# Kernel optimization log

Measured on AMD Instinct MI355X. Metric: run time of the kernel, lower is better.

Reference implementation:

```python
import jax, jax.numpy as jnp
import numpy as np

EPS_NORM = 1e-12
EPS_COS = 1e-8

def _l2norm(x, axis):
    n = jnp.linalg.norm(x, axis=axis, keepdims=True)
    return x / jnp.maximum(n, EPS_NORM)

def setup_inputs() -> dict:
    key = jax.random.key(0)
    k1, k2, k3 = jax.random.split(key, 3)
    B, C, H, W, M = 16, 512, 32, 32, 1024
    query = jax.random.normal(k1, (B, C, H, W), dtype=jnp.float32)
    keys = jax.random.normal(k2, (M, C), dtype=jnp.float32)
    entropy = jax.random.uniform(k3, (B * H * W, 1), dtype=jnp.float32) + 1e-3
    return {"query": query, "keys": keys, "entropy": entropy}

def reference(query, keys, entropy):
    B, C, H, W = query.shape
    M = keys.shape[0]
    N = B * H * W
    # F.normalize over channel dim, then BCHW -> BHWC -> [N, C]
    q = _l2norm(query, axis=1)
    q = jnp.transpose(q, (0, 2, 3, 1))
    qr = q.reshape(N, C)

    # get_score: softmax over queries (axis 0) and over memory (axis 1)
    score = jnp.einsum('nd,md->nm', qr, keys)  # [N, M]
    sq = jax.nn.softmax(score, axis=0)
    sm = jax.nn.softmax(score, axis=1)

    # ---- memory_loss ----
    argm = jnp.argmax(sm, axis=1)               # topk(k=1) over memory
    closest = keys[argm]                         # [N, C]
    eye = jnp.eye(M, dtype=keys.dtype)
    gram = keys @ keys.T
    diversity_loss = jnp.sum((gram * (1.0 - eye)) ** 2) / (M * M - M)
    cos = jnp.sum(qr * closest, axis=1) / jnp.maximum(
        jnp.linalg.norm(qr, axis=1) * jnp.linalg.norm(closest, axis=1), EPS_COS)
    similarity_loss = jnp.dot(1.0 - cos, entropy[:, 0])  # CosineEmbeddingLoss(target=1) . entropy

    # ---- read ----
    concat_memory = jax.lax.stop_gradient(sm) @ keys    # [N, C]
    updated_query = jnp.concatenate([qr, concat_memory], axis=1)  # [N, 2C]
    updated_query = updated_query.reshape(B, H, W, 2 * C)
    updated_query = jnp.transpose(updated_query, (0, 3, 1, 2))    # [B, 2C, H, W]

    # ---- update (train=True) ----
    g = argm                                     # gathering indices (argmax == topk1)
    sq_d = jax.lax.stop_gradient(sq)
    ent_d = jax.lax.stop_gradient(entropy[:, 0])
    colmax = jnp.max(sq_d, axis=0)               # max score per memory slot [M]
    w = (sq_d[jnp.arange(N), g] / colmax[g]) * (ent_d / jnp.max(ent_d))  # [N]
    query_update = jax.ops.segment_sum(w[:, None] * qr, g, num_segments=M)  # [M, C]
    updated_memory = _l2norm(query_update + jax.lax.stop_gradient(keys), axis=1)
    gram2 = updated_memory @ updated_memory.T
    diversity_loss_updated = jnp.sum((gram2 * (1.0 - eye)) ** 2) / (M * M - M)
    updated_memory = jax.lax.stop_gradient(updated_memory)

    return (updated_query, updated_memory, sq, sm, diversity_loss_updated, similarity_loss)
```

## Files before the change

kernel.cpp:

```cpp
#include <hip/hip_runtime.h>

typedef unsigned int  u32;
typedef unsigned short u16;
typedef __bf16 bf16x8 __attribute__((ext_vector_type(8)));
typedef float  f32x4  __attribute__((ext_vector_type(4)));

#define O1 16777216
#define O2 17301504
#define O3 34078720
#define O4 50855936
#define O5 50855937

#define WS_QHI   0u
#define WS_QLO   16777216u
#define WS_KHI   33554432u
#define WS_KLO   34603008u
#define WS_KT    35651584u
#define WS_KNORM 36700160u
#define WS_CNT   36704256u
#define WS_OFFS  36708352u
#define WS_CUR   36712704u
#define WS_RN    36769792u
#define WS_PMAX  36835328u
#define WS_CMAX  36966400u
#define WS_CSUM  36970496u
#define WS_ARGM  36974592u
#define WS_WGT   37040128u
#define WS_SCAL  39202816u
#define WS_PM2   39203840u
#define WS_PS2   39728128u
#define WS_SM16  40252416u

__device__ __forceinline__ u16 bf_rne(float f){
  u32 u = __float_as_uint(f);
  u32 r = u + 0x7fffu + ((u >> 16) & 1u);
  return (u16)(r >> 16);
}
__device__ __forceinline__ float bf_f(u16 h){ return __uint_as_float(((u32)h) << 16); }

__device__ __forceinline__ void glds16(const void* g, void* l){
  __builtin_amdgcn_global_load_lds((const __attribute__((address_space(1))) u32*)g,
                                   (__attribute__((address_space(3))) u32*)l, 16, 0, 0);
}

__global__ void k_init(u32* count, float* scal){
  int i = blockIdx.x*256 + threadIdx.x;
  if (i < 1024) count[i] = 0u;
  if (i < 16) scal[i] = 0.f;
}

__global__ __launch_bounds__(64) void k_keys(const float* __restrict__ keys,
    u16* __restrict__ khi, u16* __restrict__ klo, float* __restrict__ knorm){
  int m = blockIdx.x, l = threadIdx.x;
  const float* kr = keys + (size_t)m*512 + l*8;
  float f[8];
  #pragma unroll
  for (int i=0;i<8;i++) f[i] = kr[i];
  float ss = 0.f;
  #pragma unroll
  for (int i=0;i<8;i++) ss += f[i]*f[i];
  for (int o=32;o>0;o>>=1) ss += __shfl_xor(ss,o);
  if (l == 0) knorm[m] = sqrtf(ss);
  u32 hh[4], ll[4];
  #pragma unroll
  for (int i=0;i<4;i++){
    u16 h0 = bf_rne(f[2*i]);   u16 l0 = bf_rne(f[2*i]   - bf_f(h0));
    u16 h1 = bf_rne(f[2*i+1]); u16 l1 = bf_rne(f[2*i+1] - bf_f(h1));
    hh[i] = (u32)h0 | ((u32)h1<<16);
    ll[i] = (u32)l0 | ((u32)l1<<16);
  }
  *(uint4*)&khi[(size_t)m*512 + l*8] = make_uint4(hh[0],hh[1],hh[2],hh[3]);
  *(uint4*)&klo[(size_t)m*512 + l*8] = make_uint4(ll[0],ll[1],ll[2],ll[3]);
}

__global__ __launch_bounds__(256) void k_keysT(const float* __restrict__ keys, u16* __restrict__ kT){
  __shared__ float t2[64*65];
  int m0 = blockIdx.x*64, c0 = blockIdx.y*64;
  int t = threadIdx.x; int j = t & 63; int ig = t >> 6;
  #pragma unroll 4
  for (int ii=0; ii<16; ++ii){
    int i = ig*16 + ii;
    t2[i*65 + j] = keys[(size_t)(m0+i)*512 + c0 + j];
  }
  __syncthreads();
  #pragma unroll 4
  for (int ii=0; ii<16; ++ii){
    int i = ig*16 + ii;
    kT[(size_t)(c0+i)*1024 + m0 + j] = bf_rne(t2[j*65 + i]);
  }
}

__global__ __launch_bounds__(256) void k_maxent(const float* __restrict__ ent, float* scal){
  int i = blockIdx.x*512 + threadIdx.x;
  float v = fmaxf(ent[i], ent[i + 256]);
  for (int o=32;o>0;o>>=1) v = fmaxf(v, __shfl_xor(v,o));
  __shared__ float r4[4];
  if ((threadIdx.x & 63) == 0) r4[threadIdx.x>>6] = v;
  __syncthreads();
  if (threadIdx.x == 0){
    float mx = fmaxf(fmaxf(r4[0],r4[1]), fmaxf(r4[2],r4[3]));
    atomicMax((u32*)(scal + 1), __float_as_uint(mx));
  }
}

__global__ __launch_bounds__(256) void k_phaseA(const float* __restrict__ query, float* __restrict__ out0,
    u16* __restrict__ qhi, u16* __restrict__ qlo, float* __restrict__ rn_g){
  __shared__ float tile[64*65];
  __shared__ float red[256];
  __shared__ float sinv[64];
  int bx = blockIdx.x; int b = bx >> 4; int hw0 = (bx & 15)*64;
  int t = threadIdx.x; int hw = t & 63; int cg = t >> 6;
  const float* qb = query + (size_t)b*524288 + hw0 + hw;
  float p = 0.f;
  for (int c = cg; c < 512; c += 4){ float v = qb[(size_t)c*1024]; p += v*v; }
  red[cg*64 + hw] = p;
  __syncthreads();
  if (t < 64){
    float ss = red[t] + red[64+t] + red[128+t] + red[192+t];
    float nrm = sqrtf(ss);
    float inv = 1.0f / fmaxf(nrm, 1e-12f);
    sinv[t] = inv;
    rn_g[b*1024 + hw0 + t] = nrm * inv;
  }
  __syncthreads();
  int nl = t >> 2, cq = t & 3;
  int n = b*1024 + hw0 + nl;
  float invv = sinv[hw];
  for (int cb = 0; cb < 8; ++cb){
    int cbase = cb*64;
    #pragma unroll 4
    for (int i = 0; i < 16; ++i){
      int cl = cg*16 + i;
      int c = cbase + cl;
      float v = query[(size_t)b*524288 + (size_t)c*1024 + hw0 + hw] * invv;
      tile[cl*65 + hw] = v;
      out0[(size_t)b*1048576 + (size_t)c*1024 + hw0 + hw] = v;
    }
    __syncthreads();
    u32 hh[8], ll[8];
    #pragma unroll
    for (int p2 = 0; p2 < 8; ++p2){
      float f0 = tile[(cq*16 + p2*2)*65 + nl];
      float f1 = tile[(cq*16 + p2*2 + 1)*65 + nl];
      u16 h0 = bf_rne(f0); u16 lo0 = bf_rne(f0 - bf_f(h0));
      u16 h1 = bf_rne(f1); u16 lo1 = bf_rne(f1 - bf_f(h1));
      hh[p2] = (u32)h0 | ((u32)h1 << 16);
      ll[p2] = (u32)lo0 | ((u32)lo1 << 16);
    }
    size_t base = (size_t)n*512 + cbase + cq*16;
    *(uint4*)&qhi[base]     = make_uint4(hh[0],hh[1],hh[2],hh[3]);
    *(uint4*)&qhi[base + 8] = make_uint4(hh[4],hh[5],hh[6],hh[7]);
    *(uint4*)&qlo[base]     = make_uint4(ll[0],ll[1],ll[2],ll[3]);
    *(uint4*)&qlo[base + 8] = make_uint4(ll[4],ll[5],ll[6],ll[7]);
    __syncthreads();
  }
}

__global__ __launch_bounds__(256) void k_score(const u16* __restrict__ qhi, const u16* __restrict__ qlo,
    const u16* __restrict__ khi, const u16* __restrict__ klo, float* __restrict__ S,
    float* __restrict__ pm2, float* __restrict__ ps2){
  __shared__ u16 sAh[8192], sAl[8192], sBh[8192], sBl[8192];
  int tid = threadIdx.x;
  int nt = blockIdx.x >> 3, mt = blockIdx.x & 7;
  int nBase = nt*128, mBase = mt*128;
  int wave = tid >> 6, lane = tid & 63;
  int rw = (wave>>1)*64, cw = (wave&1)*64;
  int m16 = lane & 15, q4 = lane >> 4;
  f32x4 acc[4][4] = {};
  int srow = tid >> 3, sg = tid & 7;
  for (int kit = 0; kit < 8; ++kit){
    int k0 = kit*64;
    #pragma unroll
    for (int it = 0; it < 4; ++it){
      int row = it*32 + srow;
      int gsw = (sg ^ (row & 7)) * 8;
      int lo = it*2048 + tid*8;
      glds16(qhi + (size_t)(nBase + row)*512 + k0 + gsw, &sAh[lo]);
      glds16(qlo + (size_t)(nBase + row)*512 + k0 + gsw, &sAl[lo]);
      glds16(khi + (size_t)(mBase + row)*512 + k0 + gsw, &sBh[lo]);
      glds16(klo + (size_t)(mBase + row)*512 + k0 + gsw, &sBl[lo]);
    }
    __syncthreads();
    #pragma unroll
    for (int ks = 0; ks < 2; ++ks){
      bf16x8 a0[4], a1[4], b0[4], b1[4];
      int g = ks*4 + q4;
      #pragma unroll
      for (int i=0;i<4;i++){
        int r = rw + i*16 + m16;
        int off = r*64 + (g ^ (r&7))*8;
        a0[i] = *(const bf16x8*)&sAh[off];
        a1[i] = *(const bf16x8*)&sAl[off];
      }
      #pragma unroll
      for (int j=0;j<4;j++){
        int r = cw + j*16 + m16;
        int off = r*64 + (g ^ (r&7))*8;
        b0[j] = *(const bf16x8*)&sBh[off];
        b1[j] = *(const bf16x8*)&sBl[off];
      }
      #pragma unroll
      for (int i=0;i<4;i++)
        #pragma unroll
        for (int j=0;j<4;j++){
          acc[i][j] = __builtin_amdgcn_mfma_f32_16x16x32_bf16(a0[i], b0[j], acc[i][j], 0,0,0);
          acc[i][j] = __builtin_amdgcn_mfma_f32_16x16x32_bf16(a0[i], b1[j], acc[i][j], 0,0,0);
          acc[i][j] = __builtin_amdgcn_mfma_f32_16x16x32_bf16(a1[i], b0[j], acc[i][j], 0,0,0);
        }
    }
    __syncthreads();
  }
  #pragma unroll
  for (int i=0;i<4;i++){
    int rbase = nBase + rw + i*16 + q4*4;
    #pragma unroll
    for (int j=0;j<4;j++){
      int col = mBase + cw + j*16 + m16;
      #pragma unroll
      for (int r=0;r<4;r++)
        S[(size_t)(rbase + r)*1024 + col] = acc[i][j][r];
    }
  }
  float* lm = (float*)sAh;
  float* ls = lm + 256;
  #pragma unroll
  for (int j=0;j<4;j++){
    float cm = -3.4e38f;
    #pragma unroll
    for (int i=0;i<4;i++)
      #pragma unroll
      for (int r=0;r<4;r++) cm = fmaxf(cm, acc[i][j][r]);
    cm = fmaxf(cm, __shfl_xor(cm, 16));
    cm = fmaxf(cm, __shfl_xor(cm, 32));
    float cs = 0.f;
    #pragma unroll
    for (int i=0;i<4;i++)
      #pragma unroll
      for (int r=0;r<4;r++) cs += __expf(acc[i][j][r] - cm);
    cs += __shfl_xor(cs, 16);
    cs += __shfl_xor(cs, 32);
    if (lane < 16){
      lm[(wave*4 + j)*16 + m16] = cm;
      ls[(wave*4 + j)*16 + m16] = cs;
    }
  }
  __syncthreads();
  if (tid < 128){
    int w = tid >> 6;
    int x = tid & 63;
    int j = x >> 4, c16 = x & 15;
    float m0 = lm[(w*4 + j)*16 + c16],     s0 = ls[(w*4 + j)*16 + c16];
    float m1 = lm[((w+2)*4 + j)*16 + c16], s1 = ls[((w+2)*4 + j)*16 + c16];
    float M  = fmaxf(m0, m1);
    float Sv = s0*__expf(m0 - M) + s1*__expf(m1 - M);
    int col = mBase + w*64 + j*16 + c16;
    pm2[nt*1024 + col] = M;
    ps2[nt*1024 + col] = Sv;
  }
}

__global__ void k_colfin(const float* __restrict__ pm2, const float* __restrict__ ps2,
    float* __restrict__ cmax, float* __restrict__ csum){
  int col = blockIdx.x*256 + threadIdx.x;
  float M = -3.4e38f, s = 0.f;
  for (int ch=0; ch<128; ++ch){
    float mi = pm2[ch*1024 + col], si = ps2[ch*1024 + col];
    float nm = fmaxf(M, mi);
    s = s*__expf(M - nm) + si*__expf(mi - nm);
    M = nm;
  }
  cmax[col] = M; csum[col] = s;
}

__global__ __launch_bounds__(256) void k_row(float* __restrict__ S, float* __restrict__ sm,
    u16* __restrict__ sm16,
    const float* __restrict__ cmax, const float* __restrict__ csum,
    const float* __restrict__ rn, const float* __restrict__ knorm,
    const float* __restrict__ ent, const float* __restrict__ scal,
    int* __restrict__ argm, float* __restrict__ wgt, u32* __restrict__ count,
    float* __restrict__ sim_acc){
  int wave = threadIdx.x >> 6, lane = threadIdx.x & 63;
  int n = blockIdx.x*4 + wave;
  float4 v[4];
  const float4* Sr = (const float4*)(S + (size_t)n*1024);
  #pragma unroll
  for (int j=0;j<4;j++) v[j] = Sr[j*64 + lane];
  float m = -3.4e38f; int gi = 0;
  #pragma unroll
  for (int j=0;j<4;j++){
    int c0 = j*256 + lane*4;
    if (v[j].x > m){ m=v[j].x; gi=c0; }
    if (v[j].y > m){ m=v[j].y; gi=c0+1; }
    if (v[j].z > m){ m=v[j].z; gi=c0+2; }
    if (v[j].w > m){ m=v[j].w; gi=c0+3; }
  }
  for (int o=32;o>0;o>>=1){
    float om = __shfl_xor(m,o); int oi = __shfl_xor(gi,o);
    if (om > m || (om == m && oi < gi)){ m = om; gi = oi; }
  }
  float4 e[4]; float s = 0.f;
  #pragma unroll
  for (int j=0;j<4;j++){
    e[j].x = __expf(v[j].x - m); e[j].y = __expf(v[j].y - m);
    e[j].z = __expf(v[j].z - m); e[j].w = __expf(v[j].w - m);
    s += e[j].x + e[j].y + e[j].z + e[j].w;
  }
  for (int o=32;o>0;o>>=1) s += __shfl_xor(s,o);
  float ri = 1.f/s;
  float4* smr = (float4*)(sm + (size_t)n*1024);
  #pragma unroll
  for (int j=0;j<4;j++){
    float4 t2; t2.x=e[j].x*ri; t2.y=e[j].y*ri; t2.z=e[j].z*ri; t2.w=e[j].w*ri;
    smr[j*64 + lane] = t2;
    u32 w0 = (u32)bf_rne(t2.x) | ((u32)bf_rne(t2.y) << 16);
    u32 w1 = (u32)bf_rne(t2.z) | ((u32)bf_rne(t2.w) << 16);
    *(uint2*)&sm16[(size_t)n*1024 + j*256 + lane*4] = make_uint2(w0, w1);
  }
  float4* sqr = (float4*)(S + (size_t)n*1024);
  #pragma unroll
  for (int j=0;j<4;j++){
    int c0 = j*256 + lane*4;
    float4 cm = *(const float4*)(cmax + c0);
    float4 cs = *(const float4*)(csum + c0);
    float4 q;
    q.x = __expf(v[j].x - cm.x)/cs.x;
    q.y = __expf(v[j].y - cm.y)/cs.y;
    q.z = __expf(v[j].z - cm.z)/cs.z;
    q.w = __expf(v[j].w - cm.w)/cs.w;
    sqr[j*64 + lane] = q;
  }
  __shared__ float simw[4];
  if (lane == 0){
    float en = ent[n];
    float cosv = m / fmaxf(rn[n]*knorm[gi], 1e-8f);
    simw[wave] = (1.f - cosv)*en;
    float w = __expf(m - cmax[gi]) * en / scal[1];
    wgt[n] = w; argm[n] = gi;
    atomicAdd(&count[gi], 1u);
  }
  __syncthreads();
  if (threadIdx.x == 0)
    atomicAdd(sim_acc, simw[0]+simw[1]+simw[2]+simw[3]);
}

__global__ __launch_bounds__(256) void k_scan(const u32* __restrict__ count,
    u32* __restrict__ offs, u32* __restrict__ cursor){
  int t = threadIdx.x;
  u32 v0 = count[t*4], v1 = count[t*4+1], v2 = count[t*4+2], v3 = count[t*4+3];
  u32 s = v0+v1+v2+v3;
  u32 x = s;
  for (int o=1;o<64;o<<=1){ u32 y = __shfl_up(x,o); if ((t&63) >= o) x += y; }
  __shared__ u32 wsum[4];
  if ((t&63) == 63) wsum[t>>6] = x;
  __syncthreads();
  u32 wb = 0;
  for (int wv=0; wv < (t>>6); ++wv) wb += wsum[wv];
  u32 excl = wb + x - s;
  u32 o0 = excl, o1 = excl+v0, o2 = excl+v0+v1, o3 = excl+v0+v1+v2;
  offs[t*4]=o0; offs[t*4+1]=o1; offs[t*4+2]=o2; offs[t*4+3]=o3;
  cursor[t*4]=o0; cursor[t*4+1]=o1; cursor[t*4+2]=o2; cursor[t*4+3]=o3;
  if (t == 255) offs[1024] = 16384u;
}

__global__ __launch_bounds__(256) void k_bucket(const int* __restrict__ argm,
    u32* __restrict__ cursor, u32* __restrict__ list){
  int n = blockIdx.x*256 + threadIdx.x;
  int g = argm[n];
  u32 pos = atomicAdd(&cursor[g], 1u);
  list[pos] = n;
}

__global__ __launch_bounds__(128) void k_gather(const u16* __restrict__ qhi, const u16* __restrict__ qlo,
    const u32* __restrict__ offs, const u32* __restrict__ list, const float* __restrict__ wgt,
    const float* __restrict__ keys, float* __restrict__ out1, float* __restrict__ scal){
  int m = blockIdx.x, t = threadIdx.x;
  int c0 = t*4;
  float a0=0.f,a1=0.f,a2=0.f,a3=0.f;
  u32 beg = offs[m], end = offs[m+1];
  for (u32 r = beg; r < end; ++r){
    int n = (int)list[r];
    float w = wgt[n];
    uint2 hh = *(const uint2*)&qhi[(size_t)n*512 + c0];
    uint2 ll = *(const uint2*)&qlo[(size_t)n*512 + c0];
    float f0 = bf_f((u16)(hh.x & 0xffffu)) + bf_f((u16)(ll.x & 0xffffu));
    float f1 = bf_f((u16)(hh.x >> 16))     + bf_f((u16)(ll.x >> 16));
    float f2 = bf_f((u16)(hh.y & 0xffffu)) + bf_f((u16)(ll.y & 0xffffu));
    float f3 = bf_f((u16)(hh.y >> 16))     + bf_f((u16)(ll.y >> 16));
    a0 += w*f0; a1 += w*f1; a2 += w*f2; a3 += w*f3;
  }
  float4 k4 = *(const float4*)(keys + (size_t)m*512 + c0);
  float u0 = a0 + k4.x, u1 = a1 + k4.y, u2 = a2 + k4.z, u3 = a3 + k4.w;
  float ss = u0*u0 + u1*u1 + u2*u2 + u3*u3;
  for (int o=32;o>0;o>>=1) ss += __shfl_xor(ss,o);
  __shared__ float r2[2];
  if ((t&63) == 0) r2[t>>6] = ss;
  __syncthreads();
  float tot = r2[0] + r2[1];
  float inv = 1.f / fmaxf(sqrtf(tot), 1e-12f);
  float4 o4; o4.x=u0*inv; o4.y=u1*inv; o4.z=u2*inv; o4.w=u3*inv;
  *(float4*)(out1 + (size_t)m*512 + c0) = o4;
  if (t == 0){
    float s2 = tot*inv*inv;
    atomicAdd(scal + 3, s2*s2);
  }
}

__global__ __launch_bounds__(256) void k_concat(const u16* __restrict__ kT, const u16* __restrict__ sm16,
    float* __restrict__ out0){
  __shared__ u16 sA[8192];
  __shared__ u16 sB[8192];
  int tid = threadIdx.x;
  int ct = blockIdx.x & 3, nt = blockIdx.x >> 2;
  int cBase = ct*128, nBase = nt*128;
  int wave = tid>>6, lane = tid&63;
  int rw = (wave>>1)*64, cw = (wave&1)*64;
  int m16 = lane&15, q4 = lane>>4;
  f32x4 acc[4][4] = {};
  int srow = tid>>3, sg = tid&7;
  for (int kit=0; kit<16; ++kit){
    int k0 = kit*64;
    #pragma unroll
    for (int it=0; it<4; ++it){
      int row = it*32 + srow;
      int gsw = (sg ^ (row & 7)) * 8;
      int lo = it*2048 + tid*8;
      glds16(kT   + (size_t)(cBase + row)*1024 + k0 + gsw, &sA[lo]);
      glds16(sm16 + (size_t)(nBase + row)*1024 + k0 + gsw, &sB[lo]);
    }
    __syncthreads();
    #pragma unroll
    for (int ks=0; ks<2; ++ks){
      bf16x8 a[4], b[4];
      int g = ks*4 + q4;
      #pragma unroll
      for (int i=0;i<4;i++){
        int r = rw + i*16 + m16;
        a[i] = *(const bf16x8*)&sA[r*64 + (g ^ (r&7))*8];
      }
      #pragma unroll
      for (int j=0;j<4;j++){
        int r = cw + j*16 + m16;
        b[j] = *(const bf16x8*)&sB[r*64 + (g ^ (r&7))*8];
      }
      #pragma unroll
      for (int i=0;i<4;i++)
        #pragma unroll
        for (int j=0;j<4;j++)
          acc[i][j] = __builtin_amdgcn_mfma_f32_16x16x32_bf16(a[i], b[j], acc[i][j], 0,0,0);
    }
    __syncthreads();
  }
  #pragma unroll
  for (int i=0;i<4;i++){
    int c = cBase + rw + i*16 + q4*4;
    #pragma unroll
    for (int j=0;j<4;j++){
      int n = nBase + cw + j*16 + m16;
      int b2 = n >> 10, hw = n & 1023;
      #pragma unroll
      for (int r=0;r<4;r++)
        out0[(size_t)b2*1048576 + (size_t)(512 + c + r)*1024 + hw] = acc[i][j][r];
    }
  }
}

__global__ __launch_bounds__(256) void k_gram(const float* __restrict__ U, float* __restrict__ scal){
  __shared__ float Ua[64*34], Ub[64*34];
  int bx = blockIdx.x & 15, by = blockIdx.x >> 4;
  int t = threadIdx.x;
  int c1 = (t >> 4)*2, c2 = (t & 15)*2;
  float d00=0,d01=0,d10=0,d11=0;
  for (int ch=0; ch<16; ++ch){
    #pragma unroll
    for (int j=0;j<8;j++){
      int flat = j*256 + t;
      int ml = flat >> 5, c = flat & 31;
      Ua[ml*34 + c] = U[(size_t)(ch*64 + ml)*512 + bx*32 + c];
      Ub[ml*34 + c] = U[(size_t)(ch*64 + ml)*512 + by*32 + c];
    }
    __syncthreads();
    #pragma unroll 8
    for (int ml=0; ml<64; ++ml){
      float2 a = *(const float2*)&Ua[ml*34 + c1];
      float2 b = *(const float2*)&Ub[ml*34 + c2];
      d00 += a.x*b.x; d01 += a.x*b.y; d10 += a.y*b.x; d11 += a.y*b.y;
    }
    __syncthreads();
  }
  float loc = d00*d00 + d01*d01 + d10*d10 + d11*d11;
  for (int o=32;o>0;o>>=1) loc += __shfl_xor(loc,o);
  __shared__ float r4[4];
  if ((t&63) == 0) r4[t>>6] = loc;
  __syncthreads();
  if (t == 0) atomicAdd(scal + 2, r4[0]+r4[1]+r4[2]+r4[3]);
}

__global__ void k_final(const float* __restrict__ scal, float* __restrict__ out){
  out[O4] = (scal[2] - scal[3]) * (1.0f/1047552.0f);
  out[O5] = scal[0];
}

extern "C" void kernel_launch(void* const* d_in, const int* in_sizes, int n_in,
                              void* d_out, int out_size, void* d_ws, size_t ws_size,
                              hipStream_t stream) {
  const float* query = (const float*)d_in[0];
  const float* keys  = (const float*)d_in[1];
  const float* ent   = (const float*)d_in[2];
  float* out  = (float*)d_out;
  char*  ws   = (char*)d_ws;

  u16*   qhi   = (u16*)(ws + WS_QHI);
  u16*   qlo   = (u16*)(ws + WS_QLO);
  u16*   khi   = (u16*)(ws + WS_KHI);
  u16*   klo   = (u16*)(ws + WS_KLO);
  u16*   kT    = (u16*)(ws + WS_KT);
  float* knorm = (float*)(ws + WS_KNORM);
  u32*   count = (u32*)(ws + WS_CNT);
  u32*   offs  = (u32*)(ws + WS_OFFS);
  u32*   cursor= (u32*)(ws + WS_CUR);
  float* rn    = (float*)(ws + WS_RN);
  float* cmax  = (float*)(ws + WS_CMAX);
  float* csum  = (float*)(ws + WS_CSUM);
  int*   argm  = (int*)(ws + WS_ARGM);
  float* wgt   = (float*)(ws + WS_WGT);
  float* scal  = (float*)(ws + WS_SCAL);
  u32*   list  = (u32*)(ws + WS_PMAX);
  float* pm2   = (float*)(ws + WS_PM2);
  float* ps2   = (float*)(ws + WS_PS2);
  u16*   sm16  = (u16*)(ws + WS_SM16);

  float* S   = out + O2;
  float* sm  = out + O3;
  float* um  = out + O1;

  k_init   <<<4,    256, 0, stream>>>(count, scal);
  k_keys   <<<1024,  64, 0, stream>>>(keys, khi, klo, knorm);
  k_keysT  <<<dim3(16,8), 256, 0, stream>>>(keys, kT);
  k_maxent <<<32,   256, 0, stream>>>(ent, scal);
  k_phaseA <<<256,  256, 0, stream>>>(query, out, qhi, qlo, rn);
  k_score  <<<1024, 256, 0, stream>>>(qhi, qlo, khi, klo, S, pm2, ps2);
  k_colfin <<<4,    256, 0, stream>>>(pm2, ps2, cmax, csum);
  k_row    <<<4096, 256, 0, stream>>>(S, sm, sm16, cmax, csum, rn, knorm, ent, scal, argm, wgt, count, scal );
  k_scan   <<<1,    256, 0, stream>>>(count, offs, cursor);
  k_bucket <<<64,   256, 0, stream>>>(argm, cursor, list);
  k_gather <<<1024, 128, 0, stream>>>(qhi, qlo, offs, list, wgt, keys, um, scal);
  k_concat <<<512,  256, 0, stream>>>(kT, sm16, out);
  k_gram   <<<256,  256, 0, stream>>>(um, scal);
  k_final  <<<1,      1, 0, stream>>>(scal, out);
}
```

Before: 515.4 us.

## Merge preprocessing kernels, remap GEMM block order, parallelize column softmax finalize

```diff
diff --git a/kernel.cpp b/kernel.cpp
--- a/kernel.cpp
+++ b/kernel.cpp
@@ -26,6 +26,7 @@
 #define WS_CSUM  36970496u
 #define WS_ARGM  36974592u
 #define WS_WGT   37040128u
+#define WS_EMAX  37199872u
 #define WS_SCAL  39202816u
 #define WS_PM2   39203840u
 #define WS_PS2   39728128u
@@ -43,116 +44,111 @@
                                    (__attribute__((address_space(3))) u32*)l, 16, 0, 0);
 }
 
-__global__ void k_init(u32* count, float* scal){
-  int i = blockIdx.x*256 + threadIdx.x;
-  if (i < 1024) count[i] = 0u;
-  if (i < 16) scal[i] = 0.f;
-}
-
-__global__ __launch_bounds__(64) void k_keys(const float* __restrict__ keys,
-    u16* __restrict__ khi, u16* __restrict__ klo, float* __restrict__ knorm){
-  int m = blockIdx.x, l = threadIdx.x;
-  const float* kr = keys + (size_t)m*512 + l*8;
-  float f[8];
-  #pragma unroll
-  for (int i=0;i<8;i++) f[i] = kr[i];
-  float ss = 0.f;
-  #pragma unroll
-  for (int i=0;i<8;i++) ss += f[i]*f[i];
-  for (int o=32;o>0;o>>=1) ss += __shfl_xor(ss,o);
-  if (l == 0) knorm[m] = sqrtf(ss);
-  u32 hh[4], ll[4];
-  #pragma unroll
-  for (int i=0;i<4;i++){
-    u16 h0 = bf_rne(f[2*i]);   u16 l0 = bf_rne(f[2*i]   - bf_f(h0));
-    u16 h1 = bf_rne(f[2*i+1]); u16 l1 = bf_rne(f[2*i+1] - bf_f(h1));
-    hh[i] = (u32)h0 | ((u32)h1<<16);
-    ll[i] = (u32)l0 | ((u32)l1<<16);
-  }
-  *(uint4*)&khi[(size_t)m*512 + l*8] = make_uint4(hh[0],hh[1],hh[2],hh[3]);
-  *(uint4*)&klo[(size_t)m*512 + l*8] = make_uint4(ll[0],ll[1],ll[2],ll[3]);
-}
-
-__global__ __launch_bounds__(256) void k_keysT(const float* __restrict__ keys, u16* __restrict__ kT){
-  __shared__ float t2[64*65];
-  int m0 = blockIdx.x*64, c0 = blockIdx.y*64;
-  int t = threadIdx.x; int j = t & 63; int ig = t >> 6;
-  #pragma unroll 4
-  for (int ii=0; ii<16; ++ii){
-    int i = ig*16 + ii;
-    t2[i*65 + j] = keys[(size_t)(m0+i)*512 + c0 + j];
-  }
-  __syncthreads();
-  #pragma unroll 4
-  for (int ii=0; ii<16; ++ii){
-    int i = ig*16 + ii;
-    kT[(size_t)(c0+i)*1024 + m0 + j] = bf_rne(t2[j*65 + i]);
-  }
-}
-
-__global__ __launch_bounds__(256) void k_maxent(const float* __restrict__ ent, float* scal){
-  int i = blockIdx.x*512 + threadIdx.x;
-  float v = fmaxf(ent[i], ent[i + 256]);
-  for (int o=32;o>0;o>>=1) v = fmaxf(v, __shfl_xor(v,o));
-  __shared__ float r4[4];
-  if ((threadIdx.x & 63) == 0) r4[threadIdx.x>>6] = v;
-  __syncthreads();
-  if (threadIdx.x == 0){
-    float mx = fmaxf(fmaxf(r4[0],r4[1]), fmaxf(r4[2],r4[3]));
-    atomicMax((u32*)(scal + 1), __float_as_uint(mx));
-  }
-}
-
-__global__ __launch_bounds__(256) void k_phaseA(const float* __restrict__ query, float* __restrict__ out0,
+__global__ __launch_bounds__(256) void k_pre(
+    const float* __restrict__ keys, const float* __restrict__ ent,
+    const float* __restrict__ query, float* __restrict__ out0,
+    u16* __restrict__ khi, u16* __restrict__ klo, float* __restrict__ knorm,
+    u16* __restrict__ kT, float* __restrict__ emax,
     u16* __restrict__ qhi, u16* __restrict__ qlo, float* __restrict__ rn_g){
-  __shared__ float tile[64*65];
-  __shared__ float red[256];
-  __shared__ float sinv[64];
-  int bx = blockIdx.x; int b = bx >> 4; int hw0 = (bx & 15)*64;
-  int t = threadIdx.x; int hw = t & 63; int cg = t >> 6;
-  const float* qb = query + (size_t)b*524288 + hw0 + hw;
-  float p = 0.f;
-  for (int c = cg; c < 512; c += 4){ float v = qb[(size_t)c*1024]; p += v*v; }
-  red[cg*64 + hw] = p;
-  __syncthreads();
-  if (t < 64){
-    float ss = red[t] + red[64+t] + red[128+t] + red[192+t];
-    float nrm = sqrtf(ss);
-    float inv = 1.0f / fmaxf(nrm, 1e-12f);
-    sinv[t] = inv;
-    rn_g[b*1024 + hw0 + t] = nrm * inv;
-  }
-  __syncthreads();
-  int nl = t >> 2, cq = t & 3;
-  int n = b*1024 + hw0 + nl;
-  float invv = sinv[hw];
-  for (int cb = 0; cb < 8; ++cb){
-    int cbase = cb*64;
+  __shared__ float shmem[64*65 + 256 + 64];
+  float* tile = shmem;
+  float* red  = shmem + 64*65;
+  float* sinv = red + 256;
+  int bx = blockIdx.x; int t = threadIdx.x;
+
+  if (bx < 256){
+    int wave = t >> 6, l = t & 63;
+    int m = bx*4 + wave;
+    const float* kr = keys + (size_t)m*512 + l*8;
+    float f[8];
+    #pragma unroll
+    for (int i=0;i<8;i++) f[i] = kr[i];
+    float ss = 0.f;
+    #pragma unroll
+    for (int i=0;i<8;i++) ss += f[i]*f[i];
+    for (int o=32;o>0;o>>=1) ss += __shfl_xor(ss,o);
+    if (l == 0) knorm[m] = sqrtf(ss);
+    u32 hh[4], ll[4];
+    #pragma unroll
+    for (int i=0;i<4;i++){
+      u16 h0 = bf_rne(f[2*i]);   u16 l0 = bf_rne(f[2*i]   - bf_f(h0));
+      u16 h1 = bf_rne(f[2*i+1]); u16 l1 = bf_rne(f[2*i+1] - bf_f(h1));
+      hh[i] = (u32)h0 | ((u32)h1<<16);
+      ll[i] = (u32)l0 | ((u32)l1<<16);
+    }
+    *(uint4*)&khi[(size_t)m*512 + l*8] = make_uint4(hh[0],hh[1],hh[2],hh[3]);
+    *(uint4*)&klo[(size_t)m*512 + l*8] = make_uint4(ll[0],ll[1],ll[2],ll[3]);
+  } else if (bx < 384){
+    int g = bx - 256;
+    int m0 = (g & 15)*64, c0 = (g >> 4)*64;
+    int j = t & 63; int ig = t >> 6;
     #pragma unroll 4
-    for (int i = 0; i < 16; ++i){
-      int cl = cg*16 + i;
-      int c = cbase + cl;
-      float v = query[(size_t)b*524288 + (size_t)c*1024 + hw0 + hw] * invv;
-      tile[cl*65 + hw] = v;
-      out0[(size_t)b*1048576 + (size_t)c*1024 + hw0 + hw] = v;
-    }
-    __syncthreads();
-    u32 hh[8], ll[8];
-    #pragma unroll
-    for (int p2 = 0; p2 < 8; ++p2){
-      float f0 = tile[(cq*16 + p2*2)*65 + nl];
-      float f1 = tile[(cq*16 + p2*2 + 1)*65 + nl];
-      u16 h0 = bf_rne(f0); u16 lo0 = bf_rne(f0 - bf_f(h0));
-      u16 h1 = bf_rne(f1); u16 lo1 = bf_rne(f1 - bf_f(h1));
-      hh[p2] = (u32)h0 | ((u32)h1 << 16);
-      ll[p2] = (u32)lo0 | ((u32)lo1 << 16);
-    }
-    size_t base = (size_t)n*512 + cbase + cq*16;
-    *(uint4*)&qhi[base]     = make_uint4(hh[0],hh[1],hh[2],hh[3]);
-    *(uint4*)&qhi[base + 8] = make_uint4(hh[4],hh[5],hh[6],hh[7]);
-    *(uint4*)&qlo[base]     = make_uint4(ll[0],ll[1],ll[2],ll[3]);
-    *(uint4*)&qlo[base + 8] = make_uint4(ll[4],ll[5],ll[6],ll[7]);
-    __syncthreads();
+    for (int ii=0; ii<16; ++ii){
+      int i = ig*16 + ii;
+      tile[i*65 + j] = keys[(size_t)(m0+i)*512 + c0 + j];
+    }
+    __syncthreads();
+    #pragma unroll 4
+    for (int ii=0; ii<16; ++ii){
+      int i = ig*16 + ii;
+      kT[(size_t)(c0+i)*1024 + m0 + j] = bf_rne(tile[j*65 + i]);
+    }
+  } else if (bx < 416){
+    int g = bx - 384;
+    int i = g*512 + t;
+    float v = fmaxf(ent[i], ent[i + 256]);
+    for (int o=32;o>0;o>>=1) v = fmaxf(v, __shfl_xor(v,o));
+    if ((t & 63) == 0) red[t>>6] = v;
+    __syncthreads();
+    if (t == 0) emax[g] = fmaxf(fmaxf(red[0],red[1]), fmaxf(red[2],red[3]));
+  } else {
+    int bx2 = bx - 416;
+    int b = bx2 >> 4; int hw0 = (bx2 & 15)*64;
+    int hw = t & 63; int cg = t >> 6;
+    const float* qb = query + (size_t)b*524288 + hw0 + hw;
+    float p = 0.f;
+    for (int c = cg; c < 512; c += 4){ float v = qb[(size_t)c*1024]; p += v*v; }
+    red[cg*64 + hw] = p;
+    __syncthreads();
+    if (t < 64){
+      float ss = red[t] + red[64+t] + red[128+t] + red[192+t];
+      float nrm = sqrtf(ss);
+      float inv = 1.0f / fmaxf(nrm, 1e-12f);
+      sinv[t] = inv;
+      rn_g[b*1024 + hw0 + t] = nrm * inv;
+    }
+    __syncthreads();
+    int nl = t >> 2, cq = t & 3;
+    int n = b*1024 + hw0 + nl;
+    float invv = sinv[hw];
+    for (int cb = 0; cb < 8; ++cb){
+      int cbase = cb*64;
+      #pragma unroll 4
+      for (int i = 0; i < 16; ++i){
+        int cl = cg*16 + i;
+        int c = cbase + cl;
+        float v = query[(size_t)b*524288 + (size_t)c*1024 + hw0 + hw] * invv;
+        tile[cl*65 + hw] = v;
+        out0[(size_t)b*1048576 + (size_t)c*1024 + hw0 + hw] = v;
+      }
+      __syncthreads();
+      u32 hh[8], ll[8];
+      #pragma unroll
+      for (int p2 = 0; p2 < 8; ++p2){
+        float f0 = tile[(cq*16 + p2*2)*65 + nl];
+        float f1 = tile[(cq*16 + p2*2 + 1)*65 + nl];
+        u16 h0 = bf_rne(f0); u16 lo0 = bf_rne(f0 - bf_f(h0));
+        u16 h1 = bf_rne(f1); u16 lo1 = bf_rne(f1 - bf_f(h1));
+        hh[p2] = (u32)h0 | ((u32)h1 << 16);
+        ll[p2] = (u32)lo0 | ((u32)lo1 << 16);
+      }
+      size_t base = (size_t)n*512 + cbase + cq*16;
+      *(uint4*)&qhi[base]     = make_uint4(hh[0],hh[1],hh[2],hh[3]);
+      *(uint4*)&qhi[base + 8] = make_uint4(hh[4],hh[5],hh[6],hh[7]);
+      *(uint4*)&qlo[base]     = make_uint4(ll[0],ll[1],ll[2],ll[3]);
+      *(uint4*)&qlo[base + 8] = make_uint4(ll[4],ll[5],ll[6],ll[7]);
+      __syncthreads();
+    }
   }
 }
 
@@ -161,7 +157,8 @@
     float* __restrict__ pm2, float* __restrict__ ps2){
   __shared__ u16 sAh[8192], sAl[8192], sBh[8192], sBl[8192];
   int tid = threadIdx.x;
-  int nt = blockIdx.x >> 3, mt = blockIdx.x & 7;
+  int wg = ((blockIdx.x & 7) << 7) + (blockIdx.x >> 3);
+  int nt = wg >> 3, mt = wg & 7;
   int nBase = nt*128, mBase = mt*128;
   int wave = tid >> 6, lane = tid & 63;
   int rw = (wave>>1)*64, cw = (wave&1)*64;
@@ -259,17 +256,39 @@
   }
 }
 
-__global__ void k_colfin(const float* __restrict__ pm2, const float* __restrict__ ps2,
-    float* __restrict__ cmax, float* __restrict__ csum){
-  int col = blockIdx.x*256 + threadIdx.x;
+__global__ __launch_bounds__(256) void k_colfin(const float* __restrict__ pm2, const float* __restrict__ ps2,
+    float* __restrict__ cmax, float* __restrict__ csum,
+    const float* __restrict__ emax, float* __restrict__ scal, u32* __restrict__ count){
+  int bx = blockIdx.x, t = threadIdx.x;
+  if (bx < 4) count[bx*256 + t] = 0u;
+  if (bx == 4 && t == 0){
+    float mx = emax[0];
+    for (int i=1;i<32;i++) mx = fmaxf(mx, emax[i]);
+    scal[0] = 0.f; scal[1] = mx; scal[2] = 0.f; scal[3] = 0.f;
+  }
+  int col = bx*64 + (t & 63);
+  int grp = t >> 6;
   float M = -3.4e38f, s = 0.f;
-  for (int ch=0; ch<128; ++ch){
+  for (int ch = grp*32; ch < grp*32 + 32; ++ch){
     float mi = pm2[ch*1024 + col], si = ps2[ch*1024 + col];
     float nm = fmaxf(M, mi);
     s = s*__expf(M - nm) + si*__expf(mi - nm);
     M = nm;
   }
-  cmax[col] = M; csum[col] = s;
+  __shared__ float gm[256], gs[256];
+  gm[t] = M; gs[t] = s;
+  __syncthreads();
+  if (t < 64){
+    float MM = gm[t], ss2 = gs[t];
+    #pragma unroll
+    for (int g2=1; g2<4; ++g2){
+      float mi = gm[g2*64 + t], si = gs[g2*64 + t];
+      float nm = fmaxf(MM, mi);
+      ss2 = ss2*__expf(MM - nm) + si*__expf(mi - nm);
+      MM = nm;
+    }
+    cmax[col] = MM; csum[col] = ss2;
+  }
 }
 
 __global__ __launch_bounds__(256) void k_row(float* __restrict__ S, float* __restrict__ sm,
@@ -410,7 +429,8 @@
   __shared__ u16 sA[8192];
   __shared__ u16 sB[8192];
   int tid = threadIdx.x;
-  int ct = blockIdx.x & 3, nt = blockIdx.x >> 2;
+  int wg = ((blockIdx.x & 7) << 6) + (blockIdx.x >> 3);
+  int ct = wg & 3, nt = wg >> 2;
   int cBase = ct*128, nBase = nt*128;
   int wave = tid>>6, lane = tid&63;
   int rw = (wave>>1)*64, cw = (wave&1)*64;
@@ -523,6 +543,7 @@
   float* csum  = (float*)(ws + WS_CSUM);
   int*   argm  = (int*)(ws + WS_ARGM);
   float* wgt   = (float*)(ws + WS_WGT);
+  float* emax  = (float*)(ws + WS_EMAX);
   float* scal  = (float*)(ws + WS_SCAL);
   u32*   list  = (u32*)(ws + WS_PMAX);
   float* pm2   = (float*)(ws + WS_PM2);
@@ -533,13 +554,9 @@
   float* sm  = out + O3;
   float* um  = out + O1;
 
-  k_init   <<<4,    256, 0, stream>>>(count, scal);
-  k_keys   <<<1024,  64, 0, stream>>>(keys, khi, klo, knorm);
-  k_keysT  <<<dim3(16,8), 256, 0, stream>>>(keys, kT);
-  k_maxent <<<32,   256, 0, stream>>>(ent, scal);
-  k_phaseA <<<256,  256, 0, stream>>>(query, out, qhi, qlo, rn);
+  k_pre    <<<672,  256, 0, stream>>>(keys, ent, query, out, khi, klo, knorm, kT, emax, qhi, qlo, rn);
   k_score  <<<1024, 256, 0, stream>>>(qhi, qlo, khi, klo, S, pm2, ps2);
-  k_colfin <<<4,    256, 0, stream>>>(pm2, ps2, cmax, csum);
+  k_colfin <<<16,   256, 0, stream>>>(pm2, ps2, cmax, csum, emax, scal, count);
   k_row    <<<4096, 256, 0, stream>>>(S, sm, sm16, cmax, csum, rn, knorm, ent, scal, argm, wgt, count, scal );
   k_scan   <<<1,    256, 0, stream>>>(count, offs, cursor);
   k_bucket <<<64,   256, 0, stream>>>(argm, cursor, list);
```

New measurement: 489.4 us. -5.1%, faster.
